# Kernel optimization log

Hardware: AMD Instinct MI355X
Metric: run time of the kernel (lower is better)

Reference implementation:

```python
import jax, jax.numpy as jnp
import numpy as np

WS = 8      # window_size
NH = 4      # num_heads (fixed in module)

def setup_inputs() -> dict:
    key = jax.random.key(0)
    k1, k2, k3 = jax.random.split(key, 3)
    B, C, H, W = 8, 512, 128, 128
    x = jax.random.normal(k1, (B, C, H, W), dtype=jnp.float32)
    # nn.MultiheadAttention parameters (xavier-ish scale)
    w_in = jax.random.normal(k2, (3 * C, C), dtype=jnp.float32) * (1.0 / np.sqrt(C))
    b_in = jnp.zeros((3 * C,), dtype=jnp.float32)
    w_out = jax.random.normal(k3, (C, C), dtype=jnp.float32) * (1.0 / np.sqrt(C))
    b_out = jnp.zeros((C,), dtype=jnp.float32)
    return {"x": x, "w_in": w_in, "b_in": b_in, "w_out": w_out, "b_out": b_out}

def reference(x, w_in, b_in, w_out, b_out):
    B, C, H, W = x.shape
    Hw, Ww = H // WS, W // WS
    hd = C // NH
    # --- window partition: (B,C,H,W) -> (N, L, C), N = B*Hw*Ww, L = WS*WS ---
    xw = x.reshape(B, C, Hw, WS, Ww, WS)
    xw = xw.transpose(0, 2, 4, 1, 3, 5)            # (B,Hw,Ww,C,WS,WS)
    xw = xw.reshape(-1, C, WS * WS)                # (N, C, L)
    xw = xw.transpose(0, 2, 1)                     # (N, L, C)
    N, L, _ = xw.shape
    # --- fused QKV projection (torch MultiheadAttention in_proj) ---
    qkv = jnp.einsum('nlc,ec->nle', xw, w_in) + b_in   # (N, L, 3C)
    q, k, v = jnp.split(qkv, 3, axis=-1)
    q = q.reshape(N, L, NH, hd)
    k = k.reshape(N, L, NH, hd)
    v = v.reshape(N, L, NH, hd)
    scale = 1.0 / np.sqrt(hd)
    scores = jnp.einsum('nqhd,nkhd->nhqk', q, k) * scale   # (N,NH,L,L)
    attn = jax.nn.softmax(scores, axis=-1)
    ctx = jnp.einsum('nhqk,nkhd->nqhd', attn, v).reshape(N, L, C)
    out = jnp.einsum('nlc,oc->nlo', ctx, w_out) + b_out    # (N, L, C)
    # --- window merge: (N,L,C) -> (B,C,H,W) ---
    out = out.transpose(0, 2, 1)                           # (N, C, L)
    out = out.reshape(B, Hw, Ww, C, WS, WS)
    out = out.transpose(0, 3, 1, 4, 2, 5)                  # (B,C,Hw,WS,Ww,WS)
    return out.reshape(B, C, H, W)
```

## Files before the change

kernel.cpp:

```cpp
#include <hip/hip_runtime.h>


typedef __attribute__((ext_vector_type(8))) short s16x8;
typedef __attribute__((ext_vector_type(4))) float f32x4;

#define C_TOT 512
#define HWIMG 128
#define CH_STRIDE (HWIMG * HWIMG)
#define NWIN 2048
#define XW_ELEMS ((size_t)NWIN * 64 * 512)
#define XW_BYTES (XW_ELEMS * 2ull)
#define WIT_ELEMS 786432ull
#define WOT_ELEMS 262144ull
#define WBF_ELEMS 1048576ull
#define CTX_BYTES_FULL (XW_ELEMS * 2ull)

__device__ __forceinline__ unsigned short f2bf(float f) {
  unsigned u = __float_as_uint(f);
  u += 0x7FFFu + ((u >> 16) & 1u);
  return (unsigned short)(u >> 16);
}

__device__ __forceinline__ void gload_lds16(const void* g, void* l) {
  __builtin_amdgcn_global_load_lds(
      (const __attribute__((address_space(1))) unsigned int*)g,
      (__attribute__((address_space(3))) unsigned int*)l, 16, 0, 0);
}

__global__ void conv_w_kernel(const float* __restrict__ w_in,
                              const float* __restrict__ w_out,
                              unsigned short* __restrict__ wbf) {
  int i = blockIdx.x * blockDim.x + threadIdx.x;
  const int NIN = 3 * C_TOT * C_TOT;
  float v = (i < NIN) ? w_in[i] : w_out[i - NIN];
  wbf[i] = f2bf(v);
}

__global__ void __launch_bounds__(256)
conv_pack_kernel(const float* __restrict__ w_in,
                 const float* __restrict__ w_out,
                 const float* __restrict__ x,
                 unsigned short* __restrict__ wit,
                 unsigned short* __restrict__ wot,
                 unsigned short* __restrict__ xw) {
  if (blockIdx.x < 4096) {
    int i = blockIdx.x * blockDim.x + threadIdx.x;
    const int NIN = 3 * C_TOT * C_TOT;
    if (i < NIN) {
      const int e = i >> 9, c = i & 511;
      const int t = e >> 9, rem = e & 511;
      const int h = rem >> 7, d = rem & 127;
      const int m = t * 8 + (d >> 4), l = d & 15;
      const int c8 = c >> 3, ec = c & 7;
      wit[(((size_t)(h * 24 + m) * 64 + c8) << 7) + l * 8 + ec] = f2bf(w_in[i]);
    } else {
      const int j = i - NIN;
      const int od = j >> 9, c = j & 511;
      const int m = od >> 4, l = od & 15;
      const int c8 = c >> 3, ec = c & 7;
      wot[(((size_t)m * 64 + c8) << 7) + l * 8 + ec] = f2bf(w_out[j]);
    }
    return;
  }
  const int blk = blockIdx.x - 4096;
  const int bb  = blk >> 8;
  const int hw  = (blk >> 4) & 15;
  const int og4 = blk & 15;
  const int t   = threadIdx.x;
  const int p0  = 4 * t;
  const int r   = p0 >> 7;
  const int col0 = p0 & 127;
  const int n   = bb * 256 + hw * 16 + (col0 >> 3);
  const int tok0 = r * 8 + (col0 & 7);
  const float* xs = x + (size_t)bb * C_TOT * CH_STRIDE
                  + (size_t)hw * 1024 + p0;
  unsigned short* pw = xw + (size_t)n * 32768;
#pragma unroll
  for (int jo = 0; jo < 4; ++jo) {
    const int o = og4 * 4 + jo;
    float4 f[8];
#pragma unroll
    for (int k = 0; k < 8; ++k)
      f[k] = *(const float4*)(xs + (size_t)(8 * o + k) * CH_STRIDE);
#pragma unroll
    for (int i = 0; i < 4; ++i) {
      s16x8 pk;
      if (i == 0) {
        pk[0]=(short)f2bf(f[0].x); pk[1]=(short)f2bf(f[1].x); pk[2]=(short)f2bf(f[2].x); pk[3]=(short)f2bf(f[3].x);
        pk[4]=(short)f2bf(f[4].x); pk[5]=(short)f2bf(f[5].x); pk[6]=(short)f2bf(f[6].x); pk[7]=(short)f2bf(f[7].x);
      } else if (i == 1) {
        pk[0]=(short)f2bf(f[0].y); pk[1]=(short)f2bf(f[1].y); pk[2]=(short)f2bf(f[2].y); pk[3]=(short)f2bf(f[3].y);
        pk[4]=(short)f2bf(f[4].y); pk[5]=(short)f2bf(f[5].y); pk[6]=(short)f2bf(f[6].y); pk[7]=(short)f2bf(f[7].y);
      } else if (i == 2) {
        pk[0]=(short)f2bf(f[0].z); pk[1]=(short)f2bf(f[1].z); pk[2]=(short)f2bf(f[2].z); pk[3]=(short)f2bf(f[3].z);
        pk[4]=(short)f2bf(f[4].z); pk[5]=(short)f2bf(f[5].z); pk[6]=(short)f2bf(f[6].z); pk[7]=(short)f2bf(f[7].z);
      } else {
        pk[0]=(short)f2bf(f[0].w); pk[1]=(short)f2bf(f[1].w); pk[2]=(short)f2bf(f[2].w); pk[3]=(short)f2bf(f[3].w);
        pk[4]=(short)f2bf(f[4].w); pk[5]=(short)f2bf(f[5].w); pk[6]=(short)f2bf(f[6].w); pk[7]=(short)f2bf(f[7].w);
      }
      *(s16x8*)(pw + ((size_t)o * 64 + tok0 + i) * 8) = pk;
    }
  }
}

#define BQO 0
#define BKO 16384
#define BVO 32768
#define BXS 49152
#define BPO 49152
#define BSO 57344
#define BLDS 81920

__global__ void __launch_bounds__(512, 4)
qkv_attn_kernel(const unsigned short* __restrict__ xw,
                const float* __restrict__ bin,
                const unsigned short* __restrict__ wit,
                unsigned short* __restrict__ ctx,
                int n0) {
  __shared__ __align__(16) unsigned char sm[BLDS];

  const int tid  = threadIdx.x;
  const int wv   = tid >> 6;
  const int lane = tid & 63;
  const int l15  = lane & 15;
  const int qd   = lane >> 4;
  const int swA  = (l15 & 7) << 4;

  const int blk = blockIdx.x;
  const int g   = blk & 7;
  const int q   = blk >> 3;
  const int h   = q & 3;
  const int nrel = (q >> 2) * 8 + g;
  const unsigned short* xww = xw + (size_t)(n0 + nrel) * 32768;

  const float SCALE = 0.08838834764831845f;
  const float L2E   = 1.4426950408889634f;

  f32x4 acc[3][4];
#pragma unroll
  for (int a = 0; a < 3; ++a)
#pragma unroll
    for (int b2 = 0; b2 < 4; ++b2) acc[a][b2] = (f32x4){0.f, 0.f, 0.f, 0.f};

  const unsigned short* arow[3];
  int typ[3], d128s[3];
#pragma unroll
  for (int mi = 0; mi < 3; ++mi) {
    const int d0 = 48 * wv + 16 * mi;
    const int t = d0 >> 7;
    const int d128 = d0 & 127;
    typ[mi] = t; d128s[mi] = d128;
    const int m = t * 8 + (d128 >> 4);
    arow[mi] = wit + ((size_t)(h * 24 + m) << 13) + l15 * 8;
  }

#pragma unroll
  for (int p = 0; p < 2; ++p)
    gload_lds16(xww + p * 4096 + tid * 8, &sm[BXS + p * 8192 + (wv << 10)]);
  __syncthreads();

  for (int s = 0; s < 4; ++s) {
    if (s < 3) {
#pragma unroll
      for (int p = 0; p < 2; ++p)
        gload_lds16(xww + (size_t)(s + 1) * 8192 + p * 4096 + tid * 8,
                    &sm[BXS + ((s + 1) & 1) * 16384 + p * 8192 + (wv << 10)]);
    }
    const int cur = BXS + (s & 1) * 16384;
#pragma unroll
    for (int j = 0; j < 4; ++j) {
      const int c8g = 16 * s + 4 * j + qd;
      const int lb = cur + ((4 * j + qd) << 10);
      s16x8 bx[4];
#pragma unroll
      for (int ni = 0; ni < 4; ++ni)
        bx[ni] = *(const s16x8*)(&sm[lb + (16 * ni + l15) * 16]);
      s16x8 af[3];
#pragma unroll
      for (int mi = 0; mi < 3; ++mi)
        af[mi] = *(const s16x8*)(arow[mi] + ((size_t)c8g << 7));
      __builtin_amdgcn_s_setprio(1);
#pragma unroll
      for (int mi = 0; mi < 3; ++mi)
#pragma unroll
        for (int ni = 0; ni < 4; ++ni)
          acc[mi][ni] = __builtin_amdgcn_mfma_f32_16x16x32_bf16(af[mi], bx[ni], acc[mi][ni], 0, 0, 0);
      __builtin_amdgcn_s_setprio(0);
    }
    __syncthreads();
  }

#pragma unroll
  for (int mi = 0; mi < 3; ++mi) {
    const int t = typ[mi], d128 = d128s[mi];
    const int e0 = t * 512 + h * 128 + d128 + 4 * qd;
    const float bi0 = bin[e0], bi1 = bin[e0 + 1], bi2 = bin[e0 + 2], bi3 = bin[e0 + 3];
#pragma unroll
    for (int ni = 0; ni < 4; ++ni) {
      const int tok = 16 * ni + l15;
      const unsigned short h0 = f2bf(acc[mi][ni][0] + bi0);
      const unsigned short h1 = f2bf(acc[mi][ni][1] + bi1);
      const unsigned short h2 = f2bf(acc[mi][ni][2] + bi2);
      const unsigned short h3 = f2bf(acc[mi][ni][3] + bi3);
      if (t < 2) {
        const unsigned lo = (unsigned)h0 | ((unsigned)h1 << 16);
        const unsigned hi = (unsigned)h2 | ((unsigned)h3 << 16);
        const unsigned long long pk = (unsigned long long)lo | ((unsigned long long)hi << 32);
        const int base = (t == 0) ? BQO : BKO;
        *(unsigned long long*)(&sm[base + tok * 256 + ((2 * (d128 + 4 * qd)) ^ swA)]) = pk;
      } else {
        const int vd = d128 + 4 * qd;
        *(unsigned short*)(&sm[BVO + (vd    ) * 128 + ((2 * tok) ^ (((vd    ) & 7) << 4))]) = h0;
        *(unsigned short*)(&sm[BVO + (vd + 1) * 128 + ((2 * tok) ^ (((vd + 1) & 7) << 4))]) = h1;
        *(unsigned short*)(&sm[BVO + (vd + 2) * 128 + ((2 * tok) ^ (((vd + 2) & 7) << 4))]) = h2;
        *(unsigned short*)(&sm[BVO + (vd + 3) * 128 + ((2 * tok) ^ (((vd + 3) & 7) << 4))]) = h3;
      }
    }
  }
  __syncthreads();

  {
    const int mq  = wv >> 1;
    const int nk0 = (wv & 1) * 2;
    f32x4 s[2];
#pragma unroll
    for (int a = 0; a < 2; ++a) s[a] = (f32x4){0.f, 0.f, 0.f, 0.f};
    const int tqa = 16 * mq + l15;
#pragma unroll
    for (int ks = 0; ks < 4; ++ks) {
      const int c0 = 32 * ks + 8 * qd;
      const s16x8 aq = *(const s16x8*)(&sm[BQO + tqa * 256 + ((2 * c0) ^ swA)]);
      s16x8 bk[2];
#pragma unroll
      for (int j = 0; j < 2; ++j) {
        const int tka = 16 * (nk0 + j) + l15;
        bk[j] = *(const s16x8*)(&sm[BKO + tka * 256 + ((2 * c0) ^ swA)]);
      }
      __builtin_amdgcn_s_setprio(1);
#pragma unroll
      for (int j = 0; j < 2; ++j)
        s[j] = __builtin_amdgcn_mfma_f32_16x16x32_bf16(aq, bk[j], s[j], 0, 0, 0);
      __builtin_amdgcn_s_setprio(0);
    }
#pragma unroll
    for (int j = 0; j < 2; ++j)
#pragma unroll
      for (int i = 0; i < 4; ++i) {
        const int tq = 16 * mq + 4 * qd + i;
        const int tk = 16 * (nk0 + j) + l15;
        *(float*)(&sm[BSO + tq * 256 + ((4 * tk) ^ ((tq & 7) << 4))]) = s[j][i] * SCALE;
      }
  }
  __syncthreads();

#pragma unroll
  for (int half = 0; half < 2; ++half) {
    const int r = 8 * wv + 2 * qd + half;
    float v[4];
#pragma unroll
    for (int j = 0; j < 4; ++j)
      v[j] = *(const float*)(&sm[BSO + r * 256 + ((4 * (16 * j + l15)) ^ ((r & 7) << 4))]);
    float m = fmaxf(fmaxf(v[0], v[1]), fmaxf(v[2], v[3]));
#pragma unroll
    for (int d = 1; d < 16; d <<= 1) m = fmaxf(m, __shfl_xor(m, d));
    float p[4], sum = 0.f;
#pragma unroll
    for (int j = 0; j < 4; ++j) {
      p[j] = exp2f((v[j] - m) * L2E);
      sum += p[j];
    }
#pragma unroll
    for (int d = 1; d < 16; d <<= 1) sum += __shfl_xor(sum, d);
    const float rinv = 1.0f / sum;
#pragma unroll
    for (int j = 0; j < 4; ++j)
      *(unsigned short*)(&sm[BPO + r * 128 + ((2 * (16 * j + l15)) ^ ((r & 7) << 4))]) =
          f2bf(p[j] * rinv);
  }
  __syncthreads();

  {
    const int mq = wv >> 1;
    const int nb = (wv & 1) * 4;
    f32x4 cacc[4];
#pragma unroll
    for (int a = 0; a < 4; ++a) cacc[a] = (f32x4){0.f, 0.f, 0.f, 0.f};
    const int tqa = 16 * mq + l15;
#pragma unroll
    for (int ks = 0; ks < 2; ++ks) {
      const int c0 = 32 * ks + 8 * qd;
      const s16x8 ap = *(const s16x8*)(&sm[BPO + tqa * 128 + ((2 * c0) ^ swA)]);
      s16x8 bv[4];
#pragma unroll
      for (int j = 0; j < 4; ++j) {
        const int vda = 16 * (nb + j) + l15;
        bv[j] = *(const s16x8*)(&sm[BVO + vda * 128 + ((2 * c0) ^ swA)]);
      }
      __builtin_amdgcn_s_setprio(1);
#pragma unroll
      for (int j = 0; j < 4; ++j)
        cacc[j] = __builtin_amdgcn_mfma_f32_16x16x32_bf16(ap, bv[j], cacc[j], 0, 0, 0);
      __builtin_amdgcn_s_setprio(0);
    }
    unsigned short* ctxn = ctx + (size_t)nrel * 32768;
#pragma unroll
    for (int j = 0; j < 4; ++j) {
      const int vd = 16 * (nb + j) + l15;
      const int c  = h * 128 + vd;
      const int c8 = c >> 3, e = c & 7;
#pragma unroll
      for (int i = 0; i < 4; ++i) {
        const int tq = 16 * mq + 4 * qd + i;
        ctxn[((size_t)c8 * 64 + tq) * 8 + e] = f2bf(cacc[j][i]);
      }
    }
  }
}

#define OXS 0
#define OLDS 32768

__global__ void __launch_bounds__(512, 4)
outproj_kernel(const unsigned short* __restrict__ ctx,
               const unsigned short* __restrict__ wot,
               const float* __restrict__ bout,
               float* __restrict__ out, int n0) {
  __shared__ __align__(16) unsigned char sm[OLDS];

  const int tid  = threadIdx.x;
  const int wv   = tid >> 6;
  const int lane = tid & 63;
  const int l15  = lane & 15;
  const int qd   = lane >> 4;

  const int nrel = blockIdx.x;
  const int n  = n0 + nrel;
  const int bb = n >> 8, hw = (n >> 4) & 15, ww = n & 15;
  const size_t wbase = (size_t)bb * C_TOT * CH_STRIDE
                     + (size_t)(hw * 8) * HWIMG + (size_t)(ww * 8);
  const unsigned short* ctxn = ctx + (size_t)nrel * 32768;

  f32x4 oacc[4][4];
#pragma unroll
  for (int a = 0; a < 4; ++a)
#pragma unroll
    for (int b2 = 0; b2 < 4; ++b2) oacc[a][b2] = (f32x4){0.f, 0.f, 0.f, 0.f};

  const unsigned short* orow[4];
#pragma unroll
  for (int mo = 0; mo < 4; ++mo)
    orow[mo] = wot + ((size_t)(4 * wv + mo) << 13) + l15 * 8;

#pragma unroll
  for (int p = 0; p < 2; ++p)
    gload_lds16(ctxn + p * 4096 + tid * 8, &sm[OXS + p * 8192 + (wv << 10)]);
  __syncthreads();

  for (int s = 0; s < 4; ++s) {
    if (s < 3) {
#pragma unroll
      for (int p = 0; p < 2; ++p)
        gload_lds16(ctxn + (size_t)(s + 1) * 8192 + p * 4096 + tid * 8,
                    &sm[OXS + ((s + 1) & 1) * 16384 + p * 8192 + (wv << 10)]);
    }
    const int cur = OXS + (s & 1) * 16384;
#pragma unroll
    for (int j = 0; j < 4; ++j) {
      const int c8g = 16 * s + 4 * j + qd;
      const int lb = cur + ((4 * j + qd) << 10);
      s16x8 bc[4];
#pragma unroll
      for (int ni = 0; ni < 4; ++ni)
        bc[ni] = *(const s16x8*)(&sm[lb + (16 * ni + l15) * 16]);
      s16x8 af[4];
#pragma unroll
      for (int mo = 0; mo < 4; ++mo)
        af[mo] = *(const s16x8*)(orow[mo] + ((size_t)c8g << 7));
      __builtin_amdgcn_s_setprio(1);
#pragma unroll
      for (int mo = 0; mo < 4; ++mo)
#pragma unroll
        for (int ni = 0; ni < 4; ++ni)
          oacc[mo][ni] = __builtin_amdgcn_mfma_f32_16x16x32_bf16(af[mo], bc[ni], oacc[mo][ni], 0, 0, 0);
      __builtin_amdgcn_s_setprio(0);
    }
    __syncthreads();
  }

#pragma unroll
  for (int mo = 0; mo < 4; ++mo) {
    const int od0 = 64 * wv + 16 * mo + 4 * qd;
    float bo[4];
#pragma unroll
    for (int i = 0; i < 4; ++i) bo[i] = bout[od0 + i];
#pragma unroll
    for (int ni = 0; ni < 4; ++ni) {
      const int tok = 16 * ni + l15;
      const int r = tok >> 3, cc = tok & 7;
#pragma unroll
      for (int i = 0; i < 4; ++i) {
        out[wbase + (size_t)(od0 + i) * CH_STRIDE + (size_t)r * HWIMG + cc] =
            oacc[mo][ni][i] + bo[i];
      }
    }
  }
}

#define QO    0
#define KO    16384
#define VO    32768
#define PO    49152
#define CTXO  57344
#define LDSB  73728

__global__ void __launch_bounds__(256)
pack_x_fb(const float* __restrict__ x, unsigned short* __restrict__ xw) {
  const int n  = blockIdx.x;
  const int bb = n >> 8, hw = (n >> 4) & 15, ww = n & 15;
  const size_t wbase = (size_t)bb * C_TOT * CH_STRIDE
                     + (size_t)(hw * 8) * HWIMG + (size_t)(ww * 8);
  const int tok = threadIdx.x & 63;
  const int q4  = threadIdx.x >> 6;
  const int r = tok >> 3, cc = tok & 7;
  const float* px = x + wbase + (size_t)r * HWIMG + cc;
  unsigned short* pw = xw + (size_t)n * 32768;
#pragma unroll 4
  for (int j = 0; j < 16; ++j) {
    const int o = q4 * 16 + j;
    float v[8];
#pragma unroll
    for (int k = 0; k < 8; ++k) v[k] = px[(size_t)(8 * o + k) * CH_STRIDE];
    s16x8 pk;
#pragma unroll
    for (int k = 0; k < 8; ++k) pk[k] = (short)f2bf(v[k]);
    *(s16x8*)(pw + ((size_t)o * 64 + tok) * 8) = pk;
  }
}

__global__ void __launch_bounds__(512, 2)
local_attn_kernel(const unsigned short* __restrict__ xw,
                  const float* __restrict__ bin,
                  const float* __restrict__ bout,
                  const unsigned short* __restrict__ wi,
                  const unsigned short* __restrict__ wo,
                  float* __restrict__ out) {
  __shared__ __align__(16) unsigned char sm[LDSB];
  const int tid  = threadIdx.x;
  const int wv   = tid >> 6;
  const int lane = tid & 63;
  const int l15  = lane & 15;
  const int qd   = lane >> 4;
  const int swA  = (l15 & 7) << 4;
  const int n  = blockIdx.x;
  const int bb = n >> 8;
  const int hw = (n >> 4) & 15;
  const int ww = n & 15;
  const size_t wbase = (size_t)bb * C_TOT * CH_STRIDE
                     + (size_t)(hw * 8) * HWIMG + (size_t)(ww * 8);
  const unsigned short* xww = xw + (size_t)n * 32768;
  f32x4 oacc[4][4];
#pragma unroll
  for (int a = 0; a < 4; ++a)
#pragma unroll
    for (int b2 = 0; b2 < 4; ++b2) oacc[a][b2] = (f32x4){0.f, 0.f, 0.f, 0.f};
  const float SCALE = 0.08838834764831845f;
  const float L2E   = 1.4426950408889634f;
  for (int h = 0; h < 4; ++h) {
    f32x4 acc[3][4];
#pragma unroll
    for (int a = 0; a < 3; ++a)
#pragma unroll
      for (int b2 = 0; b2 < 4; ++b2) acc[a][b2] = (f32x4){0.f, 0.f, 0.f, 0.f};
    const unsigned short* arow[3];
    int typ[3], d128s[3];
#pragma unroll
    for (int mi = 0; mi < 3; ++mi) {
      const int d0 = 48 * wv + 16 * mi;
      const int t = d0 >> 7;
      const int d128 = d0 & 127;
      typ[mi] = t; d128s[mi] = d128;
      arow[mi] = wi + (size_t)(t * 512 + h * 128 + d128 + l15) * 512;
    }
#pragma unroll 4
    for (int ks = 0; ks < 16; ++ks) {
      const int c0 = 32 * ks + 8 * qd;
      const int c8 = c0 >> 3;
      s16x8 bx[4];
#pragma unroll
      for (int ni = 0; ni < 4; ++ni)
        bx[ni] = *(const s16x8*)(xww + ((size_t)c8 * 64 + 16 * ni + l15) * 8);
#pragma unroll
      for (int mi = 0; mi < 3; ++mi) {
        const s16x8 af = *(const s16x8*)(arow[mi] + c0);
#pragma unroll
        for (int ni = 0; ni < 4; ++ni)
          acc[mi][ni] = __builtin_amdgcn_mfma_f32_16x16x32_bf16(af, bx[ni], acc[mi][ni], 0, 0, 0);
      }
    }
#pragma unroll
    for (int mi = 0; mi < 3; ++mi) {
      const int t = typ[mi], d128 = d128s[mi];
      const int e0 = t * 512 + h * 128 + d128 + 4 * qd;
      const float bi0 = bin[e0], bi1 = bin[e0 + 1], bi2 = bin[e0 + 2], bi3 = bin[e0 + 3];
#pragma unroll
      for (int ni = 0; ni < 4; ++ni) {
        const int tok = 16 * ni + l15;
        const unsigned short h0 = f2bf(acc[mi][ni][0] + bi0);
        const unsigned short h1 = f2bf(acc[mi][ni][1] + bi1);
        const unsigned short h2 = f2bf(acc[mi][ni][2] + bi2);
        const unsigned short h3 = f2bf(acc[mi][ni][3] + bi3);
        if (t < 2) {
          const unsigned lo = (unsigned)h0 | ((unsigned)h1 << 16);
          const unsigned hi = (unsigned)h2 | ((unsigned)h3 << 16);
          const unsigned long long pk = (unsigned long long)lo | ((unsigned long long)hi << 32);
          const int base = (t == 0) ? QO : KO;
          *(unsigned long long*)(&sm[base + tok * 256 + ((2 * (d128 + 4 * qd)) ^ swA)]) = pk;
        } else {
          const int vd = d128 + 4 * qd;
          *(unsigned short*)(&sm[VO + (vd    ) * 128 + ((2 * tok) ^ (((vd    ) & 7) << 4))]) = h0;
          *(unsigned short*)(&sm[VO + (vd + 1) * 128 + ((2 * tok) ^ (((vd + 1) & 7) << 4))]) = h1;
          *(unsigned short*)(&sm[VO + (vd + 2) * 128 + ((2 * tok) ^ (((vd + 2) & 7) << 4))]) = h2;
          *(unsigned short*)(&sm[VO + (vd + 3) * 128 + ((2 * tok) ^ (((vd + 3) & 7) << 4))]) = h3;
        }
      }
    }
    __syncthreads();
    if (wv < 4) {
      f32x4 s[4];
#pragma unroll
      for (int a = 0; a < 4; ++a) s[a] = (f32x4){0.f, 0.f, 0.f, 0.f};
      const int tqa = 16 * wv + l15;
#pragma unroll
      for (int ks = 0; ks < 4; ++ks) {
        const int c0 = 32 * ks + 8 * qd;
        const s16x8 aq = *(const s16x8*)(&sm[QO + tqa * 256 + ((2 * c0) ^ swA)]);
#pragma unroll
        for (int ni = 0; ni < 4; ++ni) {
          const int tk = 16 * ni + l15;
          const s16x8 bk = *(const s16x8*)(&sm[KO + tk * 256 + ((2 * c0) ^ swA)]);
          s[ni] = __builtin_amdgcn_mfma_f32_16x16x32_bf16(aq, bk, s[ni], 0, 0, 0);
        }
      }
      float sv[4][4];
#pragma unroll
      for (int ni = 0; ni < 4; ++ni)
#pragma unroll
        for (int i = 0; i < 4; ++i) sv[ni][i] = s[ni][i] * SCALE;
      float m[4];
#pragma unroll
      for (int i = 0; i < 4; ++i)
        m[i] = fmaxf(fmaxf(sv[0][i], sv[1][i]), fmaxf(sv[2][i], sv[3][i]));
#pragma unroll
      for (int d = 1; d < 16; d <<= 1)
#pragma unroll
        for (int i = 0; i < 4; ++i) m[i] = fmaxf(m[i], __shfl_xor(m[i], d));
      float p[4][4], sum[4] = {0.f, 0.f, 0.f, 0.f};
#pragma unroll
      for (int ni = 0; ni < 4; ++ni)
#pragma unroll
        for (int i = 0; i < 4; ++i) {
          p[ni][i] = exp2f((sv[ni][i] - m[i]) * L2E);
          sum[i] += p[ni][i];
        }
#pragma unroll
      for (int d = 1; d < 16; d <<= 1)
#pragma unroll
        for (int i = 0; i < 4; ++i) sum[i] += __shfl_xor(sum[i], d);
      float rinv[4];
#pragma unroll
      for (int i = 0; i < 4; ++i) rinv[i] = 1.0f / sum[i];
#pragma unroll
      for (int ni = 0; ni < 4; ++ni)
#pragma unroll
        for (int i = 0; i < 4; ++i) {
          const int tqr = 16 * wv + 4 * qd + i;
          const int tk = 16 * ni + l15;
          *(unsigned short*)(&sm[PO + tqr * 128 + ((2 * tk) ^ ((tqr & 7) << 4))]) =
              f2bf(p[ni][i] * rinv[i]);
        }
    }
    __syncthreads();
    {
      const int mq = wv >> 1;
      const int nb = (wv & 1) * 4;
      f32x4 cacc[4];
#pragma unroll
      for (int a = 0; a < 4; ++a) cacc[a] = (f32x4){0.f, 0.f, 0.f, 0.f};
      const int tqa = 16 * mq + l15;
#pragma unroll
      for (int ks = 0; ks < 2; ++ks) {
        const int c0 = 32 * ks + 8 * qd;
        const s16x8 ap = *(const s16x8*)(&sm[PO + tqa * 128 + ((2 * c0) ^ swA)]);
#pragma unroll
        for (int j = 0; j < 4; ++j) {
          const int vda = 16 * (nb + j) + l15;
          const s16x8 bv = *(const s16x8*)(&sm[VO + vda * 128 + ((2 * c0) ^ swA)]);
          cacc[j] = __builtin_amdgcn_mfma_f32_16x16x32_bf16(ap, bv, cacc[j], 0, 0, 0);
        }
      }
#pragma unroll
      for (int j = 0; j < 4; ++j)
#pragma unroll
        for (int i = 0; i < 4; ++i) {
          const int tq = 16 * mq + 4 * qd + i;
          const int vd = 16 * (nb + j) + l15;
          *(unsigned short*)(&sm[CTXO + tq * 256 + ((2 * vd) ^ ((tq & 7) << 4))]) =
              f2bf(cacc[j][i]);
        }
    }
    __syncthreads();
    {
#pragma unroll
      for (int ks = 0; ks < 4; ++ks) {
        const int c0 = 32 * ks + 8 * qd;
        s16x8 a2[4];
#pragma unroll
        for (int mo = 0; mo < 4; ++mo) {
          const int od = 64 * wv + 16 * mo + l15;
          a2[mo] = *(const s16x8*)(&wo[(size_t)od * 512 + 128 * h + c0]);
        }
        s16x8 bc[4];
#pragma unroll
        for (int ni = 0; ni < 4; ++ni) {
          const int tok = 16 * ni + l15;
          bc[ni] = *(const s16x8*)(&sm[CTXO + tok * 256 + ((2 * c0) ^ swA)]);
        }
#pragma unroll
        for (int mo = 0; mo < 4; ++mo)
#pragma unroll
          for (int ni = 0; ni < 4; ++ni)
            oacc[mo][ni] = __builtin_amdgcn_mfma_f32_16x16x32_bf16(a2[mo], bc[ni], oacc[mo][ni], 0, 0, 0);
      }
    }
  }
#pragma unroll
  for (int mo = 0; mo < 4; ++mo) {
    const int od0 = 64 * wv + 16 * mo + 4 * qd;
    float bo[4];
#pragma unroll
    for (int i = 0; i < 4; ++i) bo[i] = bout[od0 + i];
#pragma unroll
    for (int ni = 0; ni < 4; ++ni) {
      const int tok = 16 * ni + l15;
      const int r = tok >> 3, cc = tok & 7;
#pragma unroll
      for (int i = 0; i < 4; ++i) {
        out[wbase + (size_t)(od0 + i) * CH_STRIDE + (size_t)r * HWIMG + cc] =
            oacc[mo][ni][i] + bo[i];
      }
    }
  }
}

extern "C" void kernel_launch(void* const* d_in, const int* in_sizes, int n_in,
                              void* d_out, int out_size, void* d_ws, size_t ws_size,
                              hipStream_t stream) {
  const float* x     = (const float*)d_in[0];
  const float* w_in  = (const float*)d_in[1];
  const float* b_in  = (const float*)d_in[2];
  const float* w_out = (const float*)d_in[3];
  const float* b_out = (const float*)d_in[4];
  float* out = (float*)d_out;

  const size_t TIL_BYTES = (WIT_ELEMS + WOT_ELEMS) * 2ull;
  int nc = 0;
  for (int c = 1; c <= 8; c <<= 1) {
    if (ws_size >= XW_BYTES + TIL_BYTES + CTX_BYTES_FULL / (size_t)c) { nc = c; break; }
  }

  if (nc) {
    unsigned short* xwp = (unsigned short*)d_ws;
    unsigned short* wit = xwp + XW_ELEMS;
    unsigned short* wot = wit + WIT_ELEMS;
    unsigned short* ctx = wot + WOT_ELEMS;
    conv_pack_kernel<<<6144, 256, 0, stream>>>(w_in, w_out, x, wit, wot, xwp);
    const int nwc = NWIN / nc;
    for (int k = 0; k < nc; ++k) {
      qkv_attn_kernel<<<nwc * 4, 512, 0, stream>>>(xwp, b_in, wit, ctx, k * nwc);
      outproj_kernel<<<nwc, 512, 0, stream>>>(ctx, wot, b_out, out, k * nwc);
    }
  } else {
    unsigned short* xwp = (unsigned short*)d_ws;
    unsigned short* wbf = xwp + XW_ELEMS;
    conv_w_kernel<<<4096, 256, 0, stream>>>(w_in, w_out, wbf);
    pack_x_fb<<<NWIN, 256, 0, stream>>>(x, xwp);
    local_attn_kernel<<<NWIN, 512, 0, stream>>>(xwp, b_in, b_out,
                                                wbf, wbf + 786432, out);
  }
}
```

Before: 540.9 us.

## Remap outproj to window strips and stage output through swizzled LDS for coalesced stores

The output-projection kernel now assigns each block a horizontal strip of 16 windows and a group of 32 output channels, with each wave covering two windows. Context operands are read straight from global memory rather than double-buffered through LDS. Results are transposed through a 64KB XOR-swizzled LDS buffer so that each output channel row is written as full 128-float image rows with float4 stores, instead of scattered 8-float segments. This targets the cost of writing the large fp32 output. In exchange, the larger LDS footprint may cut occupancy, and the ctx and weight loads are no longer staged.

```diff
diff --git a/kernel.cpp b/kernel.cpp
--- a/kernel.cpp
+++ b/kernel.cpp
@@ -317,15 +317,12 @@
   }
 }
 
-#define OXS 0
-#define OLDS 32768
-
 __global__ void __launch_bounds__(512, 4)
 outproj_kernel(const unsigned short* __restrict__ ctx,
                const unsigned short* __restrict__ wot,
                const float* __restrict__ bout,
                float* __restrict__ out, int n0) {
-  __shared__ __align__(16) unsigned char sm[OLDS];
+  __shared__ __align__(16) unsigned char sm[65536];
 
   const int tid  = threadIdx.x;
   const int wv   = tid >> 6;
@@ -333,75 +330,78 @@
   const int l15  = lane & 15;
   const int qd   = lane >> 4;
 
-  const int nrel = blockIdx.x;
-  const int n  = n0 + nrel;
-  const int bb = n >> 8, hw = (n >> 4) & 15, ww = n & 15;
-  const size_t wbase = (size_t)bb * C_TOT * CH_STRIDE
-                     + (size_t)(hw * 8) * HWIMG + (size_t)(ww * 8);
-  const unsigned short* ctxn = ctx + (size_t)nrel * 32768;
-
-  f32x4 oacc[4][4];
-#pragma unroll
-  for (int a = 0; a < 4; ++a)
-#pragma unroll
-    for (int b2 = 0; b2 < 4; ++b2) oacc[a][b2] = (f32x4){0.f, 0.f, 0.f, 0.f};
-
-  const unsigned short* orow[4];
-#pragma unroll
-  for (int mo = 0; mo < 4; ++mo)
-    orow[mo] = wot + ((size_t)(4 * wv + mo) << 13) + l15 * 8;
-
-#pragma unroll
-  for (int p = 0; p < 2; ++p)
-    gload_lds16(ctxn + p * 4096 + tid * 8, &sm[OXS + p * 8192 + (wv << 10)]);
-  __syncthreads();
-
-  for (int s = 0; s < 4; ++s) {
-    if (s < 3) {
-#pragma unroll
-      for (int p = 0; p < 2; ++p)
-        gload_lds16(ctxn + (size_t)(s + 1) * 8192 + p * 4096 + tid * 8,
-                    &sm[OXS + ((s + 1) & 1) * 16384 + p * 8192 + (wv << 10)]);
-    }
-    const int cur = OXS + (s & 1) * 16384;
-#pragma unroll
-    for (int j = 0; j < 4; ++j) {
-      const int c8g = 16 * s + 4 * j + qd;
-      const int lb = cur + ((4 * j + qd) << 10);
-      s16x8 bc[4];
-#pragma unroll
-      for (int ni = 0; ni < 4; ++ni)
-        bc[ni] = *(const s16x8*)(&sm[lb + (16 * ni + l15) * 16]);
-      s16x8 af[4];
-#pragma unroll
-      for (int mo = 0; mo < 4; ++mo)
-        af[mo] = *(const s16x8*)(orow[mo] + ((size_t)c8g << 7));
-      __builtin_amdgcn_s_setprio(1);
-#pragma unroll
-      for (int mo = 0; mo < 4; ++mo)
-#pragma unroll
-        for (int ni = 0; ni < 4; ++ni)
-          oacc[mo][ni] = __builtin_amdgcn_mfma_f32_16x16x32_bf16(af[mo], bc[ni], oacc[mo][ni], 0, 0, 0);
-      __builtin_amdgcn_s_setprio(0);
+  const int blk = blockIdx.x;
+  const int og  = blk & 15;
+  const int strip_rel = blk >> 4;
+  const int strip_g = (n0 >> 4) + strip_rel;
+  const int bb = strip_g >> 4, hw = strip_g & 15;
+  const int nrel_base = strip_g * 16 - n0;
+  const size_t sbase = (size_t)bb * C_TOT * CH_STRIDE + (size_t)hw * 1024;
+
+  f32x4 acc[2][8];
+#pragma unroll
+  for (int a = 0; a < 2; ++a)
+#pragma unroll
+    for (int b2 = 0; b2 < 8; ++b2) acc[a][b2] = (f32x4){0.f, 0.f, 0.f, 0.f};
+
+  const unsigned short* cw0 = ctx + (size_t)(nrel_base + 2 * wv) * 32768;
+  const unsigned short* cw1 = cw0 + 32768;
+  const unsigned short* ar0 = wot + ((size_t)(2 * og) << 13) + l15 * 8;
+  const unsigned short* ar1 = ar0 + 8192;
+
+#pragma unroll 2
+  for (int ks = 0; ks < 16; ++ks) {
+    const int c8g = 4 * ks + qd;
+    s16x8 bx[8];
+#pragma unroll
+    for (int t = 0; t < 4; ++t)
+      bx[t] = *(const s16x8*)(cw0 + ((size_t)c8g * 64 + 16 * t + l15) * 8);
+#pragma unroll
+    for (int t = 0; t < 4; ++t)
+      bx[4 + t] = *(const s16x8*)(cw1 + ((size_t)c8g * 64 + 16 * t + l15) * 8);
+    s16x8 af[2];
+    af[0] = *(const s16x8*)(ar0 + ((size_t)c8g << 7));
+    af[1] = *(const s16x8*)(ar1 + ((size_t)c8g << 7));
+    __builtin_amdgcn_s_setprio(1);
+#pragma unroll
+    for (int mo = 0; mo < 2; ++mo)
+#pragma unroll
+      for (int ni = 0; ni < 8; ++ni)
+        acc[mo][ni] = __builtin_amdgcn_mfma_f32_16x16x32_bf16(af[mo], bx[ni], acc[mo][ni], 0, 0, 0);
+    __builtin_amdgcn_s_setprio(0);
+  }
+
+#pragma unroll
+  for (int mo = 0; mo < 2; ++mo) {
+    if (mo) __syncthreads();
+#pragma unroll
+    for (int ni = 0; ni < 8; ++ni) {
+      const int ww = 2 * wv + (ni >> 2);
+      const int tok = ww * 64 + 16 * (ni & 3) + l15;
+#pragma unroll
+      for (int i = 0; i < 4; ++i) {
+        const int odl = 4 * qd + i;
+        *(float*)(&sm[odl * 4096 + ((tok * 4) ^ (((odl + ww) & 7) << 4))]) =
+            acc[mo][ni][i];
+      }
     }
     __syncthreads();
-  }
-
-#pragma unroll
-  for (int mo = 0; mo < 4; ++mo) {
-    const int od0 = 64 * wv + 16 * mo + 4 * qd;
-    float bo[4];
-#pragma unroll
-    for (int i = 0; i < 4; ++i) bo[i] = bout[od0 + i];
-#pragma unroll
-    for (int ni = 0; ni < 4; ++ni) {
-      const int tok = 16 * ni + l15;
-      const int r = tok >> 3, cc = tok & 7;
-#pragma unroll
-      for (int i = 0; i < 4; ++i) {
-        out[wbase + (size_t)(od0 + i) * CH_STRIDE + (size_t)r * HWIMG + cc] =
-            oacc[mo][ni][i] + bo[i];
-      }
+#pragma unroll
+    for (int k = 0; k < 8; ++k) {
+      const int u = tid + 512 * k;
+      const int odl = u >> 8;
+      const int r  = (u >> 5) & 7;
+      const int cg = u & 31;
+      const int ww = cg >> 1;
+      const int c0 = (cg & 1) * 4;
+      const int tok = ww * 64 + r * 8 + c0;
+      const f32x4 v = *(const f32x4*)(&sm[odl * 4096 + ((tok * 4) ^ (((odl + ww) & 7) << 4))]);
+      const int odg = og * 32 + mo * 16 + odl;
+      const float bo = bout[odg];
+      f32x4 vo;
+#pragma unroll
+      for (int jj = 0; jj < 4; ++jj) vo[jj] = v[jj] + bo;
+      *(f32x4*)(&out[sbase + (size_t)odg * CH_STRIDE + r * HWIMG + cg * 4]) = vo;
     }
   }
 }
```

After: 548.9 us. About the same (+1.5%).
